# Performance work log

Measured on AMD Instinct MI355X. Metric: run time of the kernel, lower is better.

Reference implementation:

```python
import jax, jax.numpy as jnp
import numpy as np

B, T, C = 4, 2048, 768
H, KVH, D = 6, 6, 128
HALF = D // 2


def setup_inputs() -> dict:
    key = jax.random.key(0)
    ks = jax.random.split(key, 5)
    x = jax.random.normal(ks[0], (B, T, C), dtype=jnp.float32)
    # true rotary frequencies
    inv_freq = 1.0 / (10000.0 ** (jnp.arange(HALF, dtype=jnp.float32) / HALF))
    ang = jnp.arange(T, dtype=jnp.float32)[:, None] * inv_freq[None, :]  # [T, HALF]
    cos, sin = jnp.cos(ang), jnp.sin(ang)
    s = 0.02
    wq = jax.random.normal(ks[1], (H * D, C), dtype=jnp.float32) * s
    wk = jax.random.normal(ks[2], (KVH * D, C), dtype=jnp.float32) * s
    wv = jax.random.normal(ks[3], (KVH * D, C), dtype=jnp.float32) * s
    wproj = jax.random.normal(ks[4], (C, C), dtype=jnp.float32) * s
    return {"x": x, "cos": cos, "sin": sin, "wq": wq, "wk": wk, "wv": wv, "wproj": wproj}


def _norm(t, eps=1e-6):
    # torch: (x - mean) / (std + eps), std unbiased (ddof=1)
    mean = jnp.mean(t, axis=-1, keepdims=True)
    var = jnp.sum((t - mean) ** 2, axis=-1, keepdims=True) / (t.shape[-1] - 1)
    return (t - mean) / (jnp.sqrt(var) + eps)


def _rope(t, cos, sin):
    # t: [B, T, heads, D]; cos/sin: [T, HALF]
    x1, x2 = t[..., :HALF], t[..., HALF:]
    c = cos[None, :, None, :]
    s = sin[None, :, None, :]
    return jnp.concatenate([x1 * c + x2 * s, -x1 * s + x2 * c], axis=-1)


def reference(x, cos, sin, wq, wk, wv, wproj):
    q = jnp.einsum('btc,oc->bto', x, wq).reshape(B, T, H, D)
    k = jnp.einsum('btc,oc->bto', x, wk).reshape(B, T, KVH, D)
    v = jnp.einsum('btc,oc->bto', x, wv).reshape(B, T, KVH, D)
    q = _norm(_rope(q, cos, sin))
    k = _norm(_rope(k, cos, sin))
    # -> [B, heads, T, D]
    q = q.transpose(0, 2, 1, 3)
    k = k.transpose(0, 2, 1, 3)
    v = v.transpose(0, 2, 1, 3)
    # nrep = H // KVH == 1, repeat_kv is a no-op here
    scale = 1.0 / jnp.sqrt(jnp.float32(D))
    scores = jnp.einsum('bhtd,bhsd->bhts', q, k) * scale  # [B,H,T,T]
    causal = jnp.tril(jnp.ones((T, T), dtype=bool))
    scores = jnp.where(causal[None, None], scores, jnp.float32(-1e30))
    attn = jax.nn.softmax(scores, axis=-1)
    y = jnp.einsum('bhts,bhsd->bhtd', attn, v)
    y = y.transpose(0, 2, 1, 3).reshape(B, T, H * D)
    return jnp.einsum('bto,co->btc', y, wproj)
```

## Files before the change

### kernel.cpp

```cpp
#include <hip/hip_runtime.h>

#define BB 4
#define TT 2048
#define CC 768
#define HH 6
#define DD 128
#define BT (BB * TT)
#define HALF 64
#define NBH (BB * HH)
#define QKSCALE 0.12753785627919282f

typedef __bf16 v8bf __attribute__((ext_vector_type(8)));
typedef float f32x4 __attribute__((ext_vector_type(4)));

__device__ __forceinline__ unsigned short f2b(float f) {
  union { float f; unsigned u; } v; v.f = f;
  unsigned r = v.u + 0x7FFFu + ((v.u >> 16) & 1u);
  return (unsigned short)(r >> 16);
}
__device__ __forceinline__ float b2f(unsigned short u) {
  union { unsigned u; float f; } v; v.u = (unsigned)u << 16;
  return v.f;
}
__device__ __forceinline__ unsigned pk2(float f0, float f1) {
  union { float f; unsigned u; } a, b; a.f = f1; b.f = f0;
  return __builtin_amdgcn_perm(a.u, b.u, 0x07060302u);
}

__device__ __forceinline__ void load_lds16(const void* g, void* l) {
  __builtin_amdgcn_global_load_lds(
      (const __attribute__((address_space(1))) unsigned int*)g,
      (__attribute__((address_space(3))) unsigned int*)(unsigned int)(unsigned long long)(l),
      16, 0, 0);
}

__global__ __launch_bounds__(256) void cvt_all_kernel(const float* __restrict__ x,
                                                      const float* __restrict__ w0,
                                                      const float* __restrict__ w1,
                                                      const float* __restrict__ w2,
                                                      const float* __restrict__ w3,
                                                      unsigned short* __restrict__ xb,
                                                      unsigned short* __restrict__ wb) {
  int bx = blockIdx.x;
  const float* src;
  unsigned short* dst;
  int i;
  if (bx < 6144) {
    src = x; dst = xb; i = bx * 256 + threadIdx.x;
  } else {
    int bsel = (bx - 6144) / 576;
    src = bsel == 0 ? w0 : bsel == 1 ? w1 : bsel == 2 ? w2 : w3;
    dst = wb + bsel * 589824;
    i = ((bx - 6144) % 576) * 256 + threadIdx.x;
  }
  float4 f = ((const float4*)src)[i];
  ushort4 o;
  o.x = f2b(f.x); o.y = f2b(f.y); o.z = f2b(f.z); o.w = f2b(f.w);
  ((ushort4*)dst)[i] = o;
}

__global__ __launch_bounds__(256) void gemm_qkv(const unsigned short* __restrict__ A,
                                                const unsigned short* __restrict__ Wall,
                                                unsigned short* __restrict__ qb,
                                                unsigned short* __restrict__ kb,
                                                unsigned short* __restrict__ vt) {
  __shared__ __align__(16) unsigned short As[2][512 * 8];
  __shared__ __align__(16) unsigned short Bs[2][512 * 8];
  const int m0 = blockIdx.x * 128;
  const int wsel = blockIdx.y / HH, h = blockIdx.y % HH;
  const unsigned short* W = Wall + (size_t)wsel * 589824 + (size_t)h * 128 * CC;
  const int tid = threadIdx.x;
  const int wave = tid >> 6, lane = tid & 63;
  const int fr = lane & 15, quad = lane >> 4;
  const int wm = (wave & 1) * 64, wn = (wave >> 1) * 64;

  f32x4 acc[4][4];
#pragma unroll
  for (int i = 0; i < 4; i++)
#pragma unroll
    for (int j = 0; j < 4; j++) acc[i][j] = (f32x4){0.f, 0.f, 0.f, 0.f};

  auto stage = [&](int kk, int buf) {
#pragma unroll
    for (int it = 0; it < 2; it++) {
      int base_slot = wave * 128 + it * 64;
      int sigma = base_slot + lane;
      int r = sigma >> 2, g = (sigma & 3) ^ ((r >> 1) & 3);
      load_lds16(A + (size_t)(m0 + r) * CC + kk + g * 8, &As[buf][base_slot * 8]);
      load_lds16(W + (size_t)r * CC + kk + g * 8, &Bs[buf][base_slot * 8]);
    }
  };

  stage(0, 0);
  __syncthreads();
  for (int step = 0; step < CC / 32; step++) {
    int buf = step & 1;
    if (step + 1 < CC / 32) stage((step + 1) * 32, buf ^ 1);
    v8bf af[4], bfr[4];
#pragma unroll
    for (int i = 0; i < 4; i++) {
      int ra = wm + i * 16 + fr;
      af[i] = *(const v8bf*)&As[buf][(4 * ra + (quad ^ ((ra >> 1) & 3))) * 8];
      int rb = wn + i * 16 + fr;
      bfr[i] = *(const v8bf*)&Bs[buf][(4 * rb + (quad ^ ((rb >> 1) & 3))) * 8];
    }
#pragma unroll
    for (int i = 0; i < 4; i++)
#pragma unroll
      for (int j = 0; j < 4; j++)
        acc[i][j] = __builtin_amdgcn_mfma_f32_16x16x32_bf16(af[i], bfr[j], acc[i][j], 0, 0, 0);
    __syncthreads();
  }

  if (wsel < 2) {
    unsigned short* dst = wsel ? kb : qb;
#pragma unroll
    for (int i = 0; i < 4; i++) {
      int rr0 = m0 + wm + i * 16 + quad * 4;
      int b = rr0 >> 11, t0 = rr0 & 2047;
      size_t base = ((size_t)(b * HH + h) * TT + t0) * DD;
#pragma unroll
      for (int j = 0; j < 4; j++) {
        int d = wn + j * 16 + fr;
#pragma unroll
        for (int r = 0; r < 4; r++)
          dst[base + (size_t)r * DD + d] = f2b(acc[i][j][r]);
      }
    }
  } else {
#pragma unroll
    for (int i = 0; i < 4; i++) {
      int rr0 = m0 + wm + i * 16 + quad * 4;
      int b = rr0 >> 11, t0 = rr0 & 2047;
      int bh = b * HH + h;
#pragma unroll
      for (int j = 0; j < 4; j++) {
        int d = wn + j * 16 + fr;
        ushort4 u = { f2b(acc[i][j][0]), f2b(acc[i][j][1]),
                      f2b(acc[i][j][2]), f2b(acc[i][j][3]) };
        *(ushort4*)&vt[((size_t)bh * DD + d) * TT + t0] = u;
      }
    }
  }
}

__global__ __launch_bounds__(256) void gemm_w64(const unsigned short* __restrict__ A,
                                                const unsigned short* __restrict__ W,
                                                float* __restrict__ C) {
  __shared__ __align__(16) unsigned short As[2][256 * 8];
  __shared__ __align__(16) unsigned short Bs[2][512 * 8];
  const int m0 = blockIdx.x * 64, n0 = blockIdx.y * 128;
  const int tid = threadIdx.x;
  const int wave = tid >> 6, lane = tid & 63;
  const int fr = lane & 15, quad = lane >> 4;
  const int wm = (wave & 1) * 32, wn = (wave >> 1) * 64;

  f32x4 acc[2][4];
#pragma unroll
  for (int i = 0; i < 2; i++)
#pragma unroll
    for (int j = 0; j < 4; j++) acc[i][j] = (f32x4){0.f, 0.f, 0.f, 0.f};

  auto stage = [&](int kk, int buf) {
    {
      int base_slot = wave * 64;
      int sigma = base_slot + lane;
      int r = sigma >> 2, g = (sigma & 3) ^ ((r >> 1) & 3);
      load_lds16(A + (size_t)(m0 + r) * CC + kk + g * 8, &As[buf][base_slot * 8]);
    }
#pragma unroll
    for (int it = 0; it < 2; it++) {
      int base_slot = wave * 128 + it * 64;
      int sigma = base_slot + lane;
      int r = sigma >> 2, g = (sigma & 3) ^ ((r >> 1) & 3);
      load_lds16(W + (size_t)(n0 + r) * CC + kk + g * 8, &Bs[buf][base_slot * 8]);
    }
  };

  stage(0, 0);
  __syncthreads();
  for (int step = 0; step < CC / 32; step++) {
    int buf = step & 1;
    if (step + 1 < CC / 32) stage((step + 1) * 32, buf ^ 1);
    v8bf af[2], bfr[4];
#pragma unroll
    for (int i = 0; i < 2; i++) {
      int ra = wm + i * 16 + fr;
      af[i] = *(const v8bf*)&As[buf][(4 * ra + (quad ^ ((ra >> 1) & 3))) * 8];
    }
#pragma unroll
    for (int j = 0; j < 4; j++) {
      int rb = wn + j * 16 + fr;
      bfr[j] = *(const v8bf*)&Bs[buf][(4 * rb + (quad ^ ((rb >> 1) & 3))) * 8];
    }
#pragma unroll
    for (int i = 0; i < 2; i++)
#pragma unroll
      for (int j = 0; j < 4; j++)
        acc[i][j] = __builtin_amdgcn_mfma_f32_16x16x32_bf16(af[i], bfr[j], acc[i][j], 0, 0, 0);
    __syncthreads();
  }

  const int orow = m0 + wm + quad * 4;
#pragma unroll
  for (int i = 0; i < 2; i++)
#pragma unroll
    for (int j = 0; j < 4; j++) {
      int oc = n0 + wn + j * 16 + fr;
#pragma unroll
      for (int r = 0; r < 4; r++)
        C[(size_t)(orow + i * 16 + r) * CC + oc] = acc[i][j][r];
    }
}

__global__ __launch_bounds__(256) void rope_all_kernel(unsigned short* __restrict__ qb,
                                                       unsigned short* __restrict__ kb,
                                                       const float* __restrict__ cosb,
                                                       const float* __restrict__ sinb) {
  int bx = blockIdx.x;
  unsigned short* qk = (bx < 12288) ? qb : kb;
  float scale = (bx < 12288) ? QKSCALE : 1.0f;
  int idx = (bx % 12288) * 4 + (threadIdx.x >> 6);
  int lane = threadIdx.x & 63;
  int tpos = idx & (TT - 1);
  size_t base = (size_t)idx * DD;

  float x1 = b2f(qk[base + lane]);
  float x2 = b2f(qk[base + HALF + lane]);
  float c = cosb[tpos * HALF + lane];
  float s = sinb[tpos * HALF + lane];
  float o1 = x1 * c + x2 * s;
  float o2 = x2 * c - x1 * s;

  float sum = o1 + o2;
#pragma unroll
  for (int off = 32; off; off >>= 1) sum += __shfl_xor(sum, off);
  float mean = sum * (1.f / 128.f);
  float d1 = o1 - mean, d2 = o2 - mean;
  float vs = d1 * d1 + d2 * d2;
#pragma unroll
  for (int off = 32; off; off >>= 1) vs += __shfl_xor(vs, off);
  float inv = scale / (sqrtf(vs * (1.f / 127.f)) + 1e-6f);

  qk[base + lane] = f2b(d1 * inv);
  qk[base + HALF + lane] = f2b(d2 * inv);
}

__global__ __launch_bounds__(256) void attn_mfma(const unsigned short* __restrict__ qtb,
                                                 const unsigned short* __restrict__ ktb,
                                                 const unsigned short* __restrict__ vtb,
                                                 unsigned short* __restrict__ Opart,
                                                 float* __restrict__ lpart) {
  __shared__ __align__(16) unsigned short Ks[2][512 * 8];
  __shared__ __align__(16) unsigned short Vts[2][512 * 8];
  __shared__ __align__(16) unsigned short Ps[4][32][40];

  const int u = blockIdx.x;
  const int bh = u % NBH;
  const int uu = u / NBH;
  int qt, c;
  if (uu < 16)      { qt = 15 - (uu >> 2); c = uu & 3; }
  else if (uu < 28) { int k = uu - 16; int q3 = k / 3; qt = 11 - q3; c = k - q3 * 3; }
  else if (uu < 36) { int k = uu - 28; qt = 7 - (k >> 1); c = k & 1; }
  else              { qt = 3 - (uu - 36); c = 0; }
  const int t0 = c * 16;
  const int t1 = min(t0 + 16, 4 * qt + 4);
  const int niter = t1 - t0;

  const int tid = threadIdx.x;
  const int wave = tid >> 6, lane = tid & 63;
  const int fr = lane & 15, quad = lane >> 4;
  const size_t head_base = (size_t)bh * TT * DD;
  const int m0 = qt * 128 + wave * 32;

  v8bf qf[2][4];
#pragma unroll
  for (int qs = 0; qs < 2; qs++)
#pragma unroll
    for (int kbk = 0; kbk < 4; kbk++)
      qf[qs][kbk] = *(const v8bf*)(qtb + head_base +
                                   (size_t)(m0 + qs * 16 + fr) * DD + kbk * 32 + quad * 8);

  const __bf16 one_bf = (__bf16)1.0f;
  v8bf ones = {one_bf, one_bf, one_bf, one_bf, one_bf, one_bf, one_bf, one_bf};

  f32x4 oacc[2][8];
#pragma unroll
  for (int qs = 0; qs < 2; qs++)
#pragma unroll
    for (int i = 0; i < 8; i++) oacc[qs][i] = (f32x4){0.f, 0.f, 0.f, 0.f};
  f32x4 lacc[2] = {(f32x4){0.f, 0.f, 0.f, 0.f}, (f32x4){0.f, 0.f, 0.f, 0.f}};

  auto stage = [&](int jt, int buf) {
    const unsigned short* kbase = ktb + head_base + (size_t)(jt * 32) * DD;
    const unsigned short* vbase = vtb + head_base + jt * 32;
#pragma unroll
    for (int it = 0; it < 2; it++) {
      int base_slot = it * 256 + wave * 64;
      int sigma = base_slot + lane;
      int s = sigma >> 4, gk = (sigma & 15) ^ (s & 7);
      load_lds16(kbase + (size_t)s * DD + gk * 8, &Ks[buf][base_slot * 8]);
      int d = sigma >> 2, gv = (sigma & 3) ^ ((d >> 1) & 3);
      load_lds16(vbase + (size_t)d * TT + gv * 8, &Vts[buf][base_slot * 8]);
    }
  };

  stage(t0, 0);
  __syncthreads();

  for (int it = 0; it < niter; it++) {
    const int jt = t0 + it;
    const int buf = it & 1;
    if (it + 1 < niter) stage(jt + 1, buf ^ 1);

    const int j0 = jt * 32;
    if (j0 <= m0 + 31) {
      f32x4 st[2][2];
#pragma unroll
      for (int qs = 0; qs < 2; qs++) { st[qs][0] = (f32x4){0,0,0,0}; st[qs][1] = (f32x4){0,0,0,0}; }
#pragma unroll
      for (int kbk = 0; kbk < 4; kbk++) {
        int g = 4 * kbk + quad;
        v8bf a0 = *(const v8bf*)&Ks[buf][(16 * fr + (g ^ (fr & 7))) * 8];
        v8bf a1 = *(const v8bf*)&Ks[buf][(16 * (fr + 16) + (g ^ (fr & 7))) * 8];
        st[0][0] = __builtin_amdgcn_mfma_f32_16x16x32_bf16(a0, qf[0][kbk], st[0][0], 0, 0, 0);
        st[0][1] = __builtin_amdgcn_mfma_f32_16x16x32_bf16(a1, qf[0][kbk], st[0][1], 0, 0, 0);
        st[1][0] = __builtin_amdgcn_mfma_f32_16x16x32_bf16(a0, qf[1][kbk], st[1][0], 0, 0, 0);
        st[1][1] = __builtin_amdgcn_mfma_f32_16x16x32_bf16(a1, qf[1][kbk], st[1][1], 0, 0, 0);
      }

      const bool diag = (j0 + 31 > m0);
#pragma unroll
      for (int qs = 0; qs < 2; qs++) {
        float p[8];
        if (diag) {
          const int qrow = m0 + qs * 16 + fr;
#pragma unroll
          for (int r = 0; r < 4; r++) {
            int c0 = j0 + quad * 4 + r;
            p[r]     = (c0      <= qrow) ? exp2f(st[qs][0][r]) : 0.f;
            p[4 + r] = (c0 + 16 <= qrow) ? exp2f(st[qs][1][r]) : 0.f;
          }
        } else {
#pragma unroll
          for (int r = 0; r < 4; r++) { p[r] = exp2f(st[qs][0][r]); p[4 + r] = exp2f(st[qs][1][r]); }
        }
        uint2 w0 = { pk2(p[0], p[1]), pk2(p[2], p[3]) };
        uint2 w1 = { pk2(p[4], p[5]), pk2(p[6], p[7]) };
        *(uint2*)&Ps[wave][qs * 16 + fr][quad * 4] = w0;
        *(uint2*)&Ps[wave][qs * 16 + fr][16 + quad * 4] = w1;
      }

      v8bf pa0 = *(const v8bf*)&Ps[wave][fr][quad * 8];
      v8bf pa1 = *(const v8bf*)&Ps[wave][16 + fr][quad * 8];
#pragma unroll
      for (int nt2 = 0; nt2 < 8; nt2++) {
        int d = nt2 * 16 + fr;
        v8bf vb = *(const v8bf*)&Vts[buf][(4 * d + (quad ^ ((d >> 1) & 3))) * 8];
        oacc[0][nt2] = __builtin_amdgcn_mfma_f32_16x16x32_bf16(pa0, vb, oacc[0][nt2], 0, 0, 0);
        oacc[1][nt2] = __builtin_amdgcn_mfma_f32_16x16x32_bf16(pa1, vb, oacc[1][nt2], 0, 0, 0);
      }
      lacc[0] = __builtin_amdgcn_mfma_f32_16x16x32_bf16(pa0, ones, lacc[0], 0, 0, 0);
      lacc[1] = __builtin_amdgcn_mfma_f32_16x16x32_bf16(pa1, ones, lacc[1], 0, 0, 0);
    }
    __syncthreads();
  }

  unsigned short* Oc = Opart + (size_t)c * (NBH * TT * DD) + head_base;
#pragma unroll
  for (int qs = 0; qs < 2; qs++) {
#pragma unroll
    for (int nt2 = 0; nt2 < 8; nt2++)
#pragma unroll
      for (int r = 0; r < 4; r++)
        Oc[(size_t)(m0 + qs * 16 + quad * 4 + r) * DD + nt2 * 16 + fr] = f2b(oacc[qs][nt2][r]);
    if (fr == 0) {
#pragma unroll
      for (int r = 0; r < 4; r++)
        lpart[c * (NBH * TT) + bh * TT + m0 + qs * 16 + quad * 4 + r] = lacc[qs][r];
    }
  }
}

__global__ __launch_bounds__(256) void combine_kernel(const unsigned short* __restrict__ Opart,
                                                      const float* __restrict__ lpart,
                                                      unsigned short* __restrict__ yb) {
  int idx = blockIdx.x * 256 + threadIdx.x;
  int row = idx >> 5;
  int dg = (idx & 31) * 4;
  int t = row & 2047;
  int qt = t >> 7;
  int nc = (4 * qt + 4 + 15) >> 4;

  float a0 = 0.f, a1 = 0.f, a2 = 0.f, a3 = 0.f, l = 0.f;
  for (int cchunk = 0; cchunk < nc; cchunk++) {
    ushort4 o = *(const ushort4*)&Opart[(size_t)cchunk * (NBH * TT * DD) + (size_t)row * DD + dg];
    a0 += b2f(o.x); a1 += b2f(o.y); a2 += b2f(o.z); a3 += b2f(o.w);
    l += lpart[cchunk * (NBH * TT) + row];
  }
  float linv = 1.f / l;
  int bh = row >> 11;
  int b = bh / HH, h = bh % HH;
  ushort4 u = { f2b(a0 * linv), f2b(a1 * linv), f2b(a2 * linv), f2b(a3 * linv) };
  *(ushort4*)&yb[((size_t)(b * TT + t)) * CC + h * DD + dg] = u;
}

extern "C" void kernel_launch(void* const* d_in, const int* in_sizes, int n_in,
                              void* d_out, int out_size, void* d_ws, size_t ws_size,
                              hipStream_t stream) {
  const float* x     = (const float*)d_in[0];
  const float* cosb  = (const float*)d_in[1];
  const float* sinb  = (const float*)d_in[2];
  const float* wq    = (const float*)d_in[3];
  const float* wk    = (const float*)d_in[4];
  const float* wv    = (const float*)d_in[5];
  const float* wproj = (const float*)d_in[6];
  float* out = (float*)d_out;

  char* w = (char*)d_ws;
  unsigned short* q_t   = (unsigned short*)(w);
  unsigned short* k_t   = (unsigned short*)(w + 12582912);
  unsigned short* v_t   = (unsigned short*)(w + 25165824);
  unsigned short* yb    = (unsigned short*)(w + 37748736);
  unsigned short* xb    = (unsigned short*)(w + 50331648);
  float*          lpart = (float*)(w + 50331648);
  unsigned short* wb    = (unsigned short*)(w + 62914560);
  unsigned short* Opart = (unsigned short*)(w + 67633152);

  cvt_all_kernel<<<8448, 256, 0, stream>>>(x, wq, wk, wv, wproj, xb, wb);

  gemm_qkv<<<dim3(BT / 128, 3 * HH), 256, 0, stream>>>(xb, wb, q_t, k_t, v_t);

  rope_all_kernel<<<24576, 256, 0, stream>>>(q_t, k_t, cosb, sinb);

  attn_mfma<<<960, 256, 0, stream>>>(q_t, k_t, v_t, Opart, lpart);
  combine_kernel<<<6144, 256, 0, stream>>>(Opart, lpart, yb);

  gemm_w64<<<dim3(BT / 64, CC / 128), 256, 0, stream>>>(yb, wb + 3 * 589824, out);
}
```

Measured before the change: 244.4 us.

## Fuse RoPE+norm into QKV GEMM epilogue and pass P via shuffles in attention

The separate rope/normalize kernel is removed. For the Q and K heads the GEMM instead computes the transposed tile, so each wave holds full 128-wide rows and applies RoPE, mean/std normalization and the scale in registers before writing bf16. In attention, the P tile is redistributed across lanes with shuffles instead of a round trip through LDS. The row sum is accumulated in scalar registers rather than through an extra MFMA with a ones vector. Block-to-head mapping is also reordered and launch bounds set to 4 waves per SIMD, trading more shuffle/VALU work and register pressure for fewer kernel launches and less memory traffic.

New measurement: 246.4 us. Within noise of the previous version (+0.8%).

```diff
diff --git a/kernel.cpp b/kernel.cpp
--- a/kernel.cpp
+++ b/kernel.cpp
@@ -61,6 +61,8 @@
 
 __global__ __launch_bounds__(256) void gemm_qkv(const unsigned short* __restrict__ A,
                                                 const unsigned short* __restrict__ Wall,
+                                                const float* __restrict__ cosb,
+                                                const float* __restrict__ sinb,
                                                 unsigned short* __restrict__ qb,
                                                 unsigned short* __restrict__ kb,
                                                 unsigned short* __restrict__ vt) {
@@ -72,13 +74,10 @@
   const int tid = threadIdx.x;
   const int wave = tid >> 6, lane = tid & 63;
   const int fr = lane & 15, quad = lane >> 4;
-  const int wm = (wave & 1) * 64, wn = (wave >> 1) * 64;
-
-  f32x4 acc[4][4];
-#pragma unroll
-  for (int i = 0; i < 4; i++)
-#pragma unroll
-    for (int j = 0; j < 4; j++) acc[i][j] = (f32x4){0.f, 0.f, 0.f, 0.f};
+
+  f32x4 acc[16];
+#pragma unroll
+  for (int i = 0; i < 16; i++) acc[i] = (f32x4){0.f, 0.f, 0.f, 0.f};
 
   auto stage = [&](int kk, int buf) {
 #pragma unroll
@@ -93,51 +92,108 @@
 
   stage(0, 0);
   __syncthreads();
-  for (int step = 0; step < CC / 32; step++) {
-    int buf = step & 1;
-    if (step + 1 < CC / 32) stage((step + 1) * 32, buf ^ 1);
-    v8bf af[4], bfr[4];
-#pragma unroll
-    for (int i = 0; i < 4; i++) {
-      int ra = wm + i * 16 + fr;
-      af[i] = *(const v8bf*)&As[buf][(4 * ra + (quad ^ ((ra >> 1) & 3))) * 8];
-      int rb = wn + i * 16 + fr;
-      bfr[i] = *(const v8bf*)&Bs[buf][(4 * rb + (quad ^ ((rb >> 1) & 3))) * 8];
-    }
-#pragma unroll
-    for (int i = 0; i < 4; i++)
-#pragma unroll
-      for (int j = 0; j < 4; j++)
-        acc[i][j] = __builtin_amdgcn_mfma_f32_16x16x32_bf16(af[i], bfr[j], acc[i][j], 0, 0, 0);
-    __syncthreads();
-  }
 
   if (wsel < 2) {
+    for (int step = 0; step < CC / 32; step++) {
+      int buf = step & 1;
+      if (step + 1 < CC / 32) stage((step + 1) * 32, buf ^ 1);
+      v8bf af[8], bfr[2];
+#pragma unroll
+      for (int i = 0; i < 8; i++) {
+        int ra = i * 16 + fr;
+        af[i] = *(const v8bf*)&Bs[buf][(4 * ra + (quad ^ ((ra >> 1) & 3))) * 8];
+      }
+#pragma unroll
+      for (int j = 0; j < 2; j++) {
+        int rb = wave * 32 + j * 16 + fr;
+        bfr[j] = *(const v8bf*)&As[buf][(4 * rb + (quad ^ ((rb >> 1) & 3))) * 8];
+      }
+#pragma unroll
+      for (int i = 0; i < 8; i++)
+#pragma unroll
+        for (int j = 0; j < 2; j++)
+          acc[i * 2 + j] = __builtin_amdgcn_mfma_f32_16x16x32_bf16(af[i], bfr[j], acc[i * 2 + j], 0, 0, 0);
+      __syncthreads();
+    }
+
     unsigned short* dst = wsel ? kb : qb;
+    const float sc = wsel ? 1.0f : QKSCALE;
+#pragma unroll
+    for (int j = 0; j < 2; j++) {
+      int t = m0 + wave * 32 + j * 16 + fr;
+      int b = t >> 11, tp = t & (TT - 1);
+      float c4[4][4], s4[4][4];
+#pragma unroll
+      for (int i = 0; i < 4; i++) {
+        *(float4*)c4[i] = *(const float4*)&cosb[tp * HALF + i * 16 + quad * 4];
+        *(float4*)s4[i] = *(const float4*)&sinb[tp * HALF + i * 16 + quad * 4];
+      }
+      float o1[4][4], o2[4][4];
+      float sum = 0.f;
+#pragma unroll
+      for (int i = 0; i < 4; i++)
+#pragma unroll
+        for (int r = 0; r < 4; r++) {
+          float x1 = acc[i * 2 + j][r], x2 = acc[(i + 4) * 2 + j][r];
+          o1[i][r] = x1 * c4[i][r] + x2 * s4[i][r];
+          o2[i][r] = x2 * c4[i][r] - x1 * s4[i][r];
+          sum += o1[i][r] + o2[i][r];
+        }
+      sum += __shfl_xor(sum, 16);
+      sum += __shfl_xor(sum, 32);
+      float mean = sum * (1.f / 128.f);
+      float vs = 0.f;
+#pragma unroll
+      for (int i = 0; i < 4; i++)
+#pragma unroll
+        for (int r = 0; r < 4; r++) {
+          float d1 = o1[i][r] - mean, d2 = o2[i][r] - mean;
+          vs += d1 * d1 + d2 * d2;
+        }
+      vs += __shfl_xor(vs, 16);
+      vs += __shfl_xor(vs, 32);
+      float inv = sc / (sqrtf(vs * (1.f / 127.f)) + 1e-6f);
+      size_t base = ((size_t)(b * HH + h) * TT + tp) * DD + quad * 4;
+#pragma unroll
+      for (int i = 0; i < 4; i++) {
+        ushort4 u1 = { f2b((o1[i][0] - mean) * inv), f2b((o1[i][1] - mean) * inv),
+                       f2b((o1[i][2] - mean) * inv), f2b((o1[i][3] - mean) * inv) };
+        *(ushort4*)&dst[base + i * 16] = u1;
+        ushort4 u2 = { f2b((o2[i][0] - mean) * inv), f2b((o2[i][1] - mean) * inv),
+                       f2b((o2[i][2] - mean) * inv), f2b((o2[i][3] - mean) * inv) };
+        *(ushort4*)&dst[base + 64 + i * 16] = u2;
+      }
+    }
+  } else {
+    const int wm = (wave & 1) * 64, wn = (wave >> 1) * 64;
+    for (int step = 0; step < CC / 32; step++) {
+      int buf = step & 1;
+      if (step + 1 < CC / 32) stage((step + 1) * 32, buf ^ 1);
+      v8bf af[4], bfr[4];
+#pragma unroll
+      for (int i = 0; i < 4; i++) {
+        int ra = wm + i * 16 + fr;
+        af[i] = *(const v8bf*)&As[buf][(4 * ra + (quad ^ ((ra >> 1) & 3))) * 8];
+        int rb = wn + i * 16 + fr;
+        bfr[i] = *(const v8bf*)&Bs[buf][(4 * rb + (quad ^ ((rb >> 1) & 3))) * 8];
+      }
+#pragma unroll
+      for (int i = 0; i < 4; i++)
+#pragma unroll
+        for (int j = 0; j < 4; j++)
+          acc[i * 4 + j] = __builtin_amdgcn_mfma_f32_16x16x32_bf16(af[i], bfr[j], acc[i * 4 + j], 0, 0, 0);
+      __syncthreads();
+    }
 #pragma unroll
     for (int i = 0; i < 4; i++) {
       int rr0 = m0 + wm + i * 16 + quad * 4;
-      int b = rr0 >> 11, t0 = rr0 & 2047;
-      size_t base = ((size_t)(b * HH + h) * TT + t0) * DD;
+      int b = rr0 >> 11, t0 = rr0 & (TT - 1);
+      int bh = b * HH + h;
 #pragma unroll
       for (int j = 0; j < 4; j++) {
         int d = wn + j * 16 + fr;
-#pragma unroll
-        for (int r = 0; r < 4; r++)
-          dst[base + (size_t)r * DD + d] = f2b(acc[i][j][r]);
-      }
-    }
-  } else {
-#pragma unroll
-    for (int i = 0; i < 4; i++) {
-      int rr0 = m0 + wm + i * 16 + quad * 4;
-      int b = rr0 >> 11, t0 = rr0 & 2047;
-      int bh = b * HH + h;
-#pragma unroll
-      for (int j = 0; j < 4; j++) {
-        int d = wn + j * 16 + fr;
-        ushort4 u = { f2b(acc[i][j][0]), f2b(acc[i][j][1]),
-                      f2b(acc[i][j][2]), f2b(acc[i][j][3]) };
+        ushort4 u = { f2b(acc[i * 4 + j][0]), f2b(acc[i * 4 + j][1]),
+                      f2b(acc[i * 4 + j][2]), f2b(acc[i * 4 + j][3]) };
         *(ushort4*)&vt[((size_t)bh * DD + d) * TT + t0] = u;
       }
     }
@@ -213,51 +269,18 @@
     }
 }
 
-__global__ __launch_bounds__(256) void rope_all_kernel(unsigned short* __restrict__ qb,
-                                                       unsigned short* __restrict__ kb,
-                                                       const float* __restrict__ cosb,
-                                                       const float* __restrict__ sinb) {
-  int bx = blockIdx.x;
-  unsigned short* qk = (bx < 12288) ? qb : kb;
-  float scale = (bx < 12288) ? QKSCALE : 1.0f;
-  int idx = (bx % 12288) * 4 + (threadIdx.x >> 6);
-  int lane = threadIdx.x & 63;
-  int tpos = idx & (TT - 1);
-  size_t base = (size_t)idx * DD;
-
-  float x1 = b2f(qk[base + lane]);
-  float x2 = b2f(qk[base + HALF + lane]);
-  float c = cosb[tpos * HALF + lane];
-  float s = sinb[tpos * HALF + lane];
-  float o1 = x1 * c + x2 * s;
-  float o2 = x2 * c - x1 * s;
-
-  float sum = o1 + o2;
-#pragma unroll
-  for (int off = 32; off; off >>= 1) sum += __shfl_xor(sum, off);
-  float mean = sum * (1.f / 128.f);
-  float d1 = o1 - mean, d2 = o2 - mean;
-  float vs = d1 * d1 + d2 * d2;
-#pragma unroll
-  for (int off = 32; off; off >>= 1) vs += __shfl_xor(vs, off);
-  float inv = scale / (sqrtf(vs * (1.f / 127.f)) + 1e-6f);
-
-  qk[base + lane] = f2b(d1 * inv);
-  qk[base + HALF + lane] = f2b(d2 * inv);
-}
-
-__global__ __launch_bounds__(256) void attn_mfma(const unsigned short* __restrict__ qtb,
-                                                 const unsigned short* __restrict__ ktb,
-                                                 const unsigned short* __restrict__ vtb,
-                                                 unsigned short* __restrict__ Opart,
-                                                 float* __restrict__ lpart) {
+__global__ __launch_bounds__(256, 4) void attn_mfma(const unsigned short* __restrict__ qtb,
+                                                    const unsigned short* __restrict__ ktb,
+                                                    const unsigned short* __restrict__ vtb,
+                                                    unsigned short* __restrict__ Opart,
+                                                    float* __restrict__ lpart) {
   __shared__ __align__(16) unsigned short Ks[2][512 * 8];
   __shared__ __align__(16) unsigned short Vts[2][512 * 8];
-  __shared__ __align__(16) unsigned short Ps[4][32][40];
-
-  const int u = blockIdx.x;
-  const int bh = u % NBH;
-  const int uu = u / NBH;
+
+  const int bid = blockIdx.x;
+  const int rest = bid >> 3;
+  const int uu = rest / 3;
+  const int bh = (rest - uu * 3) * 8 + (bid & 7);
   int qt, c;
   if (uu < 16)      { qt = 15 - (uu >> 2); c = uu & 3; }
   else if (uu < 28) { int k = uu - 16; int q3 = k / 3; qt = 11 - q3; c = k - q3 * 3; }
@@ -281,32 +304,40 @@
       qf[qs][kbk] = *(const v8bf*)(qtb + head_base +
                                    (size_t)(m0 + qs * 16 + fr) * DD + kbk * 32 + quad * 8);
 
-  const __bf16 one_bf = (__bf16)1.0f;
-  v8bf ones = {one_bf, one_bf, one_bf, one_bf, one_bf, one_bf, one_bf, one_bf};
-
   f32x4 oacc[2][8];
 #pragma unroll
   for (int qs = 0; qs < 2; qs++)
 #pragma unroll
     for (int i = 0; i < 8; i++) oacc[qs][i] = (f32x4){0.f, 0.f, 0.f, 0.f};
-  f32x4 lacc[2] = {(f32x4){0.f, 0.f, 0.f, 0.f}, (f32x4){0.f, 0.f, 0.f, 0.f}};
-
+  float lsum[2] = {0.f, 0.f};
+
+  int kslot[2], vslot[2];
+  size_t kgo[2], vgo[2];
+#pragma unroll
+  for (int it = 0; it < 2; it++) {
+    int base_slot = it * 256 + wave * 64;
+    int sigma = base_slot + lane;
+    int s = sigma >> 4, gk = (sigma & 15) ^ (s & 7);
+    kslot[it] = base_slot; kgo[it] = (size_t)s * DD + gk * 8;
+    int d = sigma >> 2, gv = (sigma & 3) ^ ((d >> 1) & 3);
+    vslot[it] = base_slot; vgo[it] = (size_t)d * TT + gv * 8;
+  }
   auto stage = [&](int jt, int buf) {
     const unsigned short* kbase = ktb + head_base + (size_t)(jt * 32) * DD;
     const unsigned short* vbase = vtb + head_base + jt * 32;
 #pragma unroll
     for (int it = 0; it < 2; it++) {
-      int base_slot = it * 256 + wave * 64;
-      int sigma = base_slot + lane;
-      int s = sigma >> 4, gk = (sigma & 15) ^ (s & 7);
-      load_lds16(kbase + (size_t)s * DD + gk * 8, &Ks[buf][base_slot * 8]);
-      int d = sigma >> 2, gv = (sigma & 3) ^ ((d >> 1) & 3);
-      load_lds16(vbase + (size_t)d * TT + gv * 8, &Vts[buf][base_slot * 8]);
+      load_lds16(kbase + kgo[it], &Ks[buf][kslot[it] * 8]);
+      load_lds16(vbase + vgo[it], &Vts[buf][vslot[it] * 8]);
     }
   };
 
   stage(t0, 0);
   __syncthreads();
+
+  const int laneA = fr + ((quad & 1) << 5);
+  const int laneB = laneA + 16;
+  const bool hiq = (quad >= 2);
 
   for (int it = 0; it < niter; it++) {
     const int jt = t0 + it;
@@ -330,6 +361,7 @@
       }
 
       const bool diag = (j0 + 31 > m0);
+      v8bf pa[2];
 #pragma unroll
       for (int qs = 0; qs < 2; qs++) {
         float p[8];
@@ -345,23 +377,29 @@
 #pragma unroll
           for (int r = 0; r < 4; r++) { p[r] = exp2f(st[qs][0][r]); p[4 + r] = exp2f(st[qs][1][r]); }
         }
-        uint2 w0 = { pk2(p[0], p[1]), pk2(p[2], p[3]) };
-        uint2 w1 = { pk2(p[4], p[5]), pk2(p[6], p[7]) };
-        *(uint2*)&Ps[wave][qs * 16 + fr][quad * 4] = w0;
-        *(uint2*)&Ps[wave][qs * 16 + fr][16 + quad * 4] = w1;
-      }
-
-      v8bf pa0 = *(const v8bf*)&Ps[wave][fr][quad * 8];
-      v8bf pa1 = *(const v8bf*)&Ps[wave][16 + fr][quad * 8];
+        lsum[qs] += ((p[0] + p[1]) + (p[2] + p[3])) + ((p[4] + p[5]) + (p[6] + p[7]));
+
+        int d0 = (int)pk2(p[0], p[1]), d1 = (int)pk2(p[2], p[3]);
+        int d2 = (int)pk2(p[4], p[5]), d3 = (int)pk2(p[6], p[7]);
+        int a0 = __shfl(d0, laneA), a1 = __shfl(d1, laneA);
+        int a2 = __shfl(d0, laneB), a3 = __shfl(d1, laneB);
+        int b0 = __shfl(d2, laneA), b1 = __shfl(d3, laneA);
+        int b2 = __shfl(d2, laneB), b3 = __shfl(d3, laneB);
+        union { uint4 u; v8bf v; } cv;
+        cv.u.x = (unsigned)(hiq ? b0 : a0);
+        cv.u.y = (unsigned)(hiq ? b1 : a1);
+        cv.u.z = (unsigned)(hiq ? b2 : a2);
+        cv.u.w = (unsigned)(hiq ? b3 : a3);
+        pa[qs] = cv.v;
+      }
+
 #pragma unroll
       for (int nt2 = 0; nt2 < 8; nt2++) {
         int d = nt2 * 16 + fr;
         v8bf vb = *(const v8bf*)&Vts[buf][(4 * d + (quad ^ ((d >> 1) & 3))) * 8];
-        oacc[0][nt2] = __builtin_amdgcn_mfma_f32_16x16x32_bf16(pa0, vb, oacc[0][nt2], 0, 0, 0);
-        oacc[1][nt2] = __builtin_amdgcn_mfma_f32_16x16x32_bf16(pa1, vb, oacc[1][nt2], 0, 0, 0);
-      }
-      lacc[0] = __builtin_amdgcn_mfma_f32_16x16x32_bf16(pa0, ones, lacc[0], 0, 0, 0);
-      lacc[1] = __builtin_amdgcn_mfma_f32_16x16x32_bf16(pa1, ones, lacc[1], 0, 0, 0);
+        oacc[0][nt2] = __builtin_amdgcn_mfma_f32_16x16x32_bf16(pa[0], vb, oacc[0][nt2], 0, 0, 0);
+        oacc[1][nt2] = __builtin_amdgcn_mfma_f32_16x16x32_bf16(pa[1], vb, oacc[1][nt2], 0, 0, 0);
+      }
     }
     __syncthreads();
   }
@@ -374,11 +412,11 @@
 #pragma unroll
       for (int r = 0; r < 4; r++)
         Oc[(size_t)(m0 + qs * 16 + quad * 4 + r) * DD + nt2 * 16 + fr] = f2b(oacc[qs][nt2][r]);
-    if (fr == 0) {
-#pragma unroll
-      for (int r = 0; r < 4; r++)
-        lpart[c * (NBH * TT) + bh * TT + m0 + qs * 16 + quad * 4 + r] = lacc[qs][r];
-    }
+    float l = lsum[qs];
+    l += __shfl_xor(l, 16);
+    l += __shfl_xor(l, 32);
+    if (quad == 0)
+      lpart[c * (NBH * TT) + bh * TT + m0 + qs * 16 + fr] = l;
   }
 }
 
@@ -429,9 +467,7 @@
 
   cvt_all_kernel<<<8448, 256, 0, stream>>>(x, wq, wk, wv, wproj, xb, wb);
 
-  gemm_qkv<<<dim3(BT / 128, 3 * HH), 256, 0, stream>>>(xb, wb, q_t, k_t, v_t);
-
-  rope_all_kernel<<<24576, 256, 0, stream>>>(q_t, k_t, cosb, sinb);
+  gemm_qkv<<<dim3(BT / 128, 3 * HH), 256, 0, stream>>>(xb, wb, cosb, sinb, q_t, k_t, v_t);
 
   attn_mfma<<<960, 256, 0, stream>>>(q_t, k_t, v_t, Opart, lpart);
   combine_kernel<<<6144, 256, 0, stream>>>(Opart, lpart, yb);
```
